# Kernel tuning notes

Hardware: AMD Instinct MI355X
Metric: run time of the kernel (lower is better)

The kernel has to match this reference:

```python
import jax, jax.numpy as jnp
import numpy as np

B, N, D, K = 16, 512, 256, 12  # batch, nodes, node_dim, num edge types (4 arg + 4 arg' + punct +/- + no_edges +/-)
ITERATION_STEPS = 1


def setup_inputs() -> dict:
    key = jax.random.key(0)
    ks = jax.random.split(key, 8)
    node = jax.random.normal(ks[0], (B, N, D), dtype=jnp.float32)
    node_mask = jax.random.randint(ks[1], (B, N), 0, 2, dtype=jnp.int32)
    graphs = jax.random.randint(ks[2], (K, B, N, N), 0, 2, dtype=jnp.int32)
    s = 1.0 / np.sqrt(D)
    Ww = jax.random.normal(ks[3], (1, D), dtype=jnp.float32) * s   # _node_weight_fc
    bw = jnp.zeros((1,), dtype=jnp.float32)
    Ws = jax.random.normal(ks[4], (D, D), dtype=jnp.float32) * s   # _self_node_fc
    bs = jnp.zeros((D,), dtype=jnp.float32)
    Wk = jax.random.normal(ks[5], (K, D, D), dtype=jnp.float32) * s  # 12 bias-free per-edge-type linears
    return {"node": node, "Ww": Ww, "bw": bw, "Ws": Ws, "bs": bs, "Wk": Wk,
            "node_mask": node_mask, "graphs": graphs}


def reference(node, Ww, bw, Ws, bs, Wk, node_mask, graphs):
    dt = node.dtype
    mask = node_mask.astype(dt)
    eye = jnp.eye(N, dtype=dt)
    # dd_graph = mask_row * mask_col * (1 - diag)
    dd = mask[:, None, :] * mask[:, :, None] * (1.0 - eye)          # [B,N,N]
    g = dd[None] * graphs.astype(dt)                                # [K,B,N,N] masked adjacencies
    neigh = g.sum(axis=(0, 3))                                      # [B,N] total neighbor count
    neigh = jnp.where(neigh >= 1, neigh, jnp.ones((), dt))

    all_w = []
    for _ in range(ITERATION_STEPS):
        # (1) node relatedness
        w = jax.nn.sigmoid(node @ Ww.T + bw)[..., 0]                # [B,N]
        all_w.append(w)
        self_info = node @ Ws.T + bs                                # [B,N,D]
        # (2) message propagation for all 12 edge types, batched
        trans = jnp.einsum('bnd,ked->kbne', node, Wk)               # [K,B,N,D] per-type linear (x @ W.T)
        wg = w[None, :, None, :] * g                                # [K,B,N,N] masked node weights
        agg = jnp.einsum('kbmn,kbnd->bmd', wg, trans) / neigh[..., None]
        # (3) update
        node = jax.nn.relu(self_info + agg)

    all_weight = jnp.stack(all_w, axis=1)                           # [B,steps,N]
    return node, all_weight
```

## Files before the change

### kernel.cpp

```cpp
#include <hip/hip_runtime.h>
#include <hip/hip_bf16.h>
#include <math.h>

#define BB 16
#define NN 512
#define DD 256
#define KK 12

typedef __bf16 bf16x8 __attribute__((ext_vector_type(8)));
typedef __bf16 bf16x4 __attribute__((ext_vector_type(4)));
typedef float  f32x4  __attribute__((ext_vector_type(4)));

#define WS_WM     0
#define WS_S      32768
#define WS_NODEBF 65536
#define WS_NODET  4259840
#define WS_WKBF   8454144
#define WS_WSBF   10027008
#define WS_T      10158080

__global__ __launch_bounds__(256) void k1_prep(const float* __restrict__ node,
        const float* __restrict__ Ww, const float* __restrict__ bw,
        const int* __restrict__ node_mask,
        float* __restrict__ wm, __bf16* __restrict__ node_bf,
        float* __restrict__ all_w) {
    int t = threadIdx.x;
    int lane = t & 63;
    int row = blockIdx.x * 4 + (t >> 6);
    const float4 nv = *(const float4*)(node + (size_t)row * DD + lane * 4);
    const float4 wv = *(const float4*)(Ww + lane * 4);
    float dot = nv.x*wv.x + nv.y*wv.y + nv.z*wv.z + nv.w*wv.w;
    #pragma unroll
    for (int off = 32; off > 0; off >>= 1) dot += __shfl_xor(dot, off);
    float w = 1.0f / (1.0f + expf(-(dot + bw[0])));
    int mk = node_mask[row];
    if (lane == 0) {
        wm[row]    = w * (float)mk;
        all_w[row] = w;
    }
    bf16x4 nb = {(__bf16)nv.x, (__bf16)nv.y, (__bf16)nv.z, (__bf16)nv.w};
    *(bf16x4*)(node_bf + (size_t)row * DD + lane * 4) = nb;
}

__global__ __launch_bounds__(256) void k1b_convert(const float* __restrict__ Wk,
        const float* __restrict__ Ws, __bf16* __restrict__ Wk_bf, __bf16* __restrict__ Ws_bf) {
    const int KDD = KK * DD * DD;
    int idx = (blockIdx.x * 256 + threadIdx.x) * 4;
    if (idx < KDD) {
        float4 v = *(const float4*)(Wk + idx);
        bf16x4 o = {(__bf16)v.x, (__bf16)v.y, (__bf16)v.z, (__bf16)v.w};
        *(bf16x4*)(Wk_bf + idx) = o;
    } else {
        int j = idx - KDD;
        if (j < DD * DD) {
            float4 v = *(const float4*)(Ws + j);
            bf16x4 o = {(__bf16)v.x, (__bf16)v.y, (__bf16)v.z, (__bf16)v.w};
            *(bf16x4*)(Ws_bf + j) = o;
        }
    }
}

__global__ __launch_bounds__(256) void k2_transpose(const __bf16* __restrict__ src,
                                                    __bf16* __restrict__ dst) {
    __shared__ __bf16 tile[64][65];
    int bx = blockIdx.x;
    int b = bx >> 5; int rest = bx & 31; int nt = rest >> 2; int dt = rest & 3;
    int n0 = nt * 64, d0 = dt * 64;
    int t = threadIdx.x;
    #pragma unroll
    for (int i = 0; i < 16; i++) {
        int idx = i * 256 + t;
        int n = idx >> 6, d = idx & 63;
        tile[n][d] = src[((size_t)(b * NN + n0 + n)) * DD + d0 + d];
    }
    __syncthreads();
    #pragma unroll
    for (int i = 0; i < 16; i++) {
        int idx = i * 256 + t;
        int d = idx >> 6, n = idx & 63;
        dst[((size_t)(b * DD + d0 + d)) * NN + n0 + n] = tile[n][d];
    }
}

__global__ __launch_bounds__(256) void k3_neigh(const int* __restrict__ graphs,
        const int* __restrict__ node_mask, float* __restrict__ s) {
    int bx = blockIdx.x;
    int b = bx >> 9, m = bx & 511;
    int t = threadIdx.x;
    int j0 = t, j1 = t + 256;
    int mk0 = (j0 != m) ? node_mask[b * NN + j0] : 0;
    int mk1 = (j1 != m) ? node_mask[b * NN + j1] : 0;
    int sum = 0;
    #pragma unroll
    for (int k = 0; k < KK; k++) {
        const int* g = graphs + ((size_t)((k * BB + b) * NN + m)) * NN;
        sum += mk0 * g[j0] + mk1 * g[j1];
    }
    #pragma unroll
    for (int off = 32; off > 0; off >>= 1) sum += __shfl_xor(sum, off);
    __shared__ int partial[4];
    if ((t & 63) == 0) partial[t >> 6] = sum;
    __syncthreads();
    if (t == 0) {
        int tot = partial[0] + partial[1] + partial[2] + partial[3];
        int mm = node_mask[b * NN + m];
        tot *= mm;
        float fn = (float)(tot >= 1 ? tot : 1);
        s[bx] = (float)mm / fn;
    }
}

__global__ __launch_bounds__(256) void k4_stageA(const int* __restrict__ graphs,
        const float* __restrict__ wm, const __bf16* __restrict__ node_t,
        __bf16* __restrict__ T) {
    __shared__ __align__(16) __bf16 Asub[64][72];
    __shared__ __align__(16) __bf16 Bsub[256][72];
    int bx = blockIdx.x;
    int mt = bx & 7;
    int kb = bx >> 3;
    int b = kb & 15;
    int k = kb >> 4;
    int m0 = mt * 64;
    int t = threadIdx.x;
    int lane = t & 63;
    int wave = t >> 6;
    int q = lane >> 4;
    int l16 = lane & 15;

    f32x4 acc[4][4];
    #pragma unroll
    for (int i = 0; i < 4; i++)
        #pragma unroll
        for (int j = 0; j < 4; j++) acc[i][j] = (f32x4){0.f, 0.f, 0.f, 0.f};

    int am = t >> 2;
    int aq = t & 3;
    const int* grow = graphs + ((size_t)((k * BB + b) * NN + m0 + am)) * NN;
    int mg = m0 + am;
    int bd = t >> 2;
    int bq = t & 3;

    for (int n0 = 0; n0 < NN; n0 += 64) {
        #pragma unroll
        for (int i = 0; i < 4; i++) {
            int nbase = n0 + aq * 16 + i * 4;
            int4 g = *(const int4*)(grow + nbase);
            float4 w4 = *(const float4*)(wm + b * NN + nbase);
            __bf16 v0 = (__bf16)((nbase + 0 != mg) ? (float)g.x * w4.x : 0.0f);
            __bf16 v1 = (__bf16)((nbase + 1 != mg) ? (float)g.y * w4.y : 0.0f);
            __bf16 v2 = (__bf16)((nbase + 2 != mg) ? (float)g.z * w4.z : 0.0f);
            __bf16 v3 = (__bf16)((nbase + 3 != mg) ? (float)g.w * w4.w : 0.0f);
            bf16x4 pack = {v0, v1, v2, v3};
            *(bf16x4*)&Asub[am][aq * 16 + i * 4] = pack;
        }
        #pragma unroll
        for (int p = 0; p < 4; p++) {
            int d = bd + p * 64;
            const __bf16* src = node_t + ((size_t)(b * DD + d)) * NN + n0 + bq * 16;
            bf16x8 u0 = *(const bf16x8*)(src);
            bf16x8 u1 = *(const bf16x8*)(src + 8);
            *(bf16x8*)&Bsub[d][bq * 16]     = u0;
            *(bf16x8*)&Bsub[d][bq * 16 + 8] = u1;
        }
        __syncthreads();
        bf16x8 af[4][2], bfr[4][2];
        #pragma unroll
        for (int fm = 0; fm < 4; fm++)
            #pragma unroll
            for (int kk = 0; kk < 2; kk++)
                af[fm][kk] = *(const bf16x8*)&Asub[fm * 16 + l16][kk * 32 + q * 8];
        #pragma unroll
        for (int fd = 0; fd < 4; fd++)
            #pragma unroll
            for (int kk = 0; kk < 2; kk++)
                bfr[fd][kk] = *(const bf16x8*)&Bsub[wave * 64 + fd * 16 + l16][kk * 32 + q * 8];
        #pragma unroll
        for (int fm = 0; fm < 4; fm++)
            #pragma unroll
            for (int fd = 0; fd < 4; fd++)
                #pragma unroll
                for (int kk = 0; kk < 2; kk++)
                    acc[fm][fd] = __builtin_amdgcn_mfma_f32_16x16x32_bf16(
                        af[fm][kk], bfr[fd][kk], acc[fm][fd], 0, 0, 0);
        __syncthreads();
    }
    #pragma unroll
    for (int fm = 0; fm < 4; fm++)
        #pragma unroll
        for (int fd = 0; fd < 4; fd++) {
            int col = wave * 64 + fd * 16 + l16;
            #pragma unroll
            for (int r = 0; r < 4; r++) {
                int m = m0 + fm * 16 + q * 4 + r;
                T[((size_t)((k * BB + b) * NN + m)) * DD + col] = (__bf16)acc[fm][fd][r];
            }
        }
}

__global__ __launch_bounds__(256) void k5_stageB(const __bf16* __restrict__ T,
        const __bf16* __restrict__ Wk_bf, const __bf16* __restrict__ node_bf,
        const __bf16* __restrict__ Ws_bf, const float* __restrict__ bs,
        const float* __restrict__ s, float* __restrict__ out) {
    __shared__ __align__(16) __bf16 AT[32][72];
    __shared__ __align__(16) __bf16 BW[256][72];
    int bx = blockIdx.x;
    int b = bx >> 4;
    int m0 = (bx & 15) * 32;
    int t = threadIdx.x;
    int lane = t & 63;
    int wave = t >> 6;
    int q = lane >> 4;
    int l16 = lane & 15;

    f32x4 acc[2][4];
    #pragma unroll
    for (int i = 0; i < 2; i++)
        #pragma unroll
        for (int j = 0; j < 4; j++) acc[i][j] = (f32x4){0.f, 0.f, 0.f, 0.f};

    int atm = t >> 3; int atc = (t & 7) * 8;
    int bwd = t >> 2; int bwc = (t & 3) * 16;

    for (int k = 0; k < KK; k++) {
        for (int et = 0; et < 4; et++) {
            int e0 = et * 64;
            *(bf16x8*)&AT[atm][atc] =
                *(const bf16x8*)(T + ((size_t)((k * BB + b) * NN + m0 + atm)) * DD + e0 + atc);
            #pragma unroll
            for (int p = 0; p < 4; p++) {
                int d = bwd + p * 64;
                const __bf16* srcp = Wk_bf + ((size_t)(k * DD + d)) * DD + e0 + bwc;
                *(bf16x8*)&BW[d][bwc]     = *(const bf16x8*)(srcp);
                *(bf16x8*)&BW[d][bwc + 8] = *(const bf16x8*)(srcp + 8);
            }
            __syncthreads();
            bf16x8 af[2][2], bfr[4][2];
            #pragma unroll
            for (int fm = 0; fm < 2; fm++)
                #pragma unroll
                for (int kk = 0; kk < 2; kk++)
                    af[fm][kk] = *(const bf16x8*)&AT[fm * 16 + l16][kk * 32 + q * 8];
            #pragma unroll
            for (int fd = 0; fd < 4; fd++)
                #pragma unroll
                for (int kk = 0; kk < 2; kk++)
                    bfr[fd][kk] = *(const bf16x8*)&BW[wave * 64 + fd * 16 + l16][kk * 32 + q * 8];
            #pragma unroll
            for (int fm = 0; fm < 2; fm++)
                #pragma unroll
                for (int fd = 0; fd < 4; fd++)
                    #pragma unroll
                    for (int kk = 0; kk < 2; kk++)
                        acc[fm][fd] = __builtin_amdgcn_mfma_f32_16x16x32_bf16(
                            af[fm][kk], bfr[fd][kk], acc[fm][fd], 0, 0, 0);
            __syncthreads();
        }
    }
    #pragma unroll
    for (int fm = 0; fm < 2; fm++) {
        float sv[4];
        #pragma unroll
        for (int r = 0; r < 4; r++) sv[r] = s[b * NN + m0 + fm * 16 + q * 4 + r];
        #pragma unroll
        for (int fd = 0; fd < 4; fd++)
            #pragma unroll
            for (int r = 0; r < 4; r++) acc[fm][fd][r] *= sv[r];
    }
    for (int et = 0; et < 4; et++) {
        int e0 = et * 64;
        *(bf16x8*)&AT[atm][atc] =
            *(const bf16x8*)(node_bf + ((size_t)(b * NN + m0 + atm)) * DD + e0 + atc);
        #pragma unroll
        for (int p = 0; p < 4; p++) {
            int d = bwd + p * 64;
            const __bf16* srcp = Ws_bf + (size_t)d * DD + e0 + bwc;
            *(bf16x8*)&BW[d][bwc]     = *(const bf16x8*)(srcp);
            *(bf16x8*)&BW[d][bwc + 8] = *(const bf16x8*)(srcp + 8);
        }
        __syncthreads();
        bf16x8 af[2][2], bfr[4][2];
        #pragma unroll
        for (int fm = 0; fm < 2; fm++)
            #pragma unroll
            for (int kk = 0; kk < 2; kk++)
                af[fm][kk] = *(const bf16x8*)&AT[fm * 16 + l16][kk * 32 + q * 8];
        #pragma unroll
        for (int fd = 0; fd < 4; fd++)
            #pragma unroll
            for (int kk = 0; kk < 2; kk++)
                bfr[fd][kk] = *(const bf16x8*)&BW[wave * 64 + fd * 16 + l16][kk * 32 + q * 8];
        #pragma unroll
        for (int fm = 0; fm < 2; fm++)
            #pragma unroll
            for (int fd = 0; fd < 4; fd++)
                #pragma unroll
                for (int kk = 0; kk < 2; kk++)
                    acc[fm][fd] = __builtin_amdgcn_mfma_f32_16x16x32_bf16(
                        af[fm][kk], bfr[fd][kk], acc[fm][fd], 0, 0, 0);
        __syncthreads();
    }
    #pragma unroll
    for (int fm = 0; fm < 2; fm++)
        #pragma unroll
        for (int fd = 0; fd < 4; fd++) {
            int col = wave * 64 + fd * 16 + l16;
            float bsv = bs[col];
            #pragma unroll
            for (int r = 0; r < 4; r++) {
                int m = m0 + fm * 16 + q * 4 + r;
                float v = acc[fm][fd][r] + bsv;
                out[((size_t)(b * NN + m)) * DD + col] = fmaxf(v, 0.0f);
            }
        }
}

extern "C" void kernel_launch(void* const* d_in, const int* in_sizes, int n_in,
                              void* d_out, int out_size, void* d_ws, size_t ws_size,
                              hipStream_t stream) {
    const float* node      = (const float*)d_in[0];
    const float* Ww        = (const float*)d_in[1];
    const float* bw        = (const float*)d_in[2];
    const float* Ws        = (const float*)d_in[3];
    const float* bs        = (const float*)d_in[4];
    const float* Wk        = (const float*)d_in[5];
    const int*   node_mask = (const int*)d_in[6];
    const int*   graphs    = (const int*)d_in[7];
    float* out   = (float*)d_out;
    float* all_w = out + (size_t)BB * NN * DD;

    char* ws = (char*)d_ws;
    float*  wm      = (float*)(ws + WS_WM);
    float*  sbuf    = (float*)(ws + WS_S);
    __bf16* node_bf = (__bf16*)(ws + WS_NODEBF);
    __bf16* node_t  = (__bf16*)(ws + WS_NODET);
    __bf16* Wk_bf   = (__bf16*)(ws + WS_WKBF);
    __bf16* Ws_bf   = (__bf16*)(ws + WS_WSBF);
    __bf16* Tbuf    = (__bf16*)(ws + WS_T);

    k1_prep    <<<2048, 256, 0, stream>>>(node, Ww, bw, node_mask, wm, node_bf, all_w);
    k1b_convert<<< 832, 256, 0, stream>>>(Wk, Ws, Wk_bf, Ws_bf);
    k2_transpose<<<512, 256, 0, stream>>>(node_bf, node_t);
    k3_neigh   <<<8192, 256, 0, stream>>>(graphs, node_mask, sbuf);
    k4_stageA  <<<1536, 256, 0, stream>>>(graphs, wm, node_t, Tbuf);
    k5_stageB  <<< 256, 256, 0, stream>>>(Tbuf, Wk_bf, node_bf, Ws_bf, bs, sbuf, out);
}
```

Measured before the change: 424.6 us.

## Fuse neighbor counting into stage A and retile stage B over contiguous K·D

Removes the separate neighbor-count kernel, which re-read the full int32 graphs tensor. Stage A now counts masked neighbors while it already loads the adjacency rows, treating a nonzero masked node weight as the column mask, and accumulates the counts with atomics into a zeroed buffer. The intermediate T is stored as [b, m, k, d] so stage B can reduce over one contiguous K·D axis with larger 64x128 tiles and a 2x2 wave split. This adds a memset, atomics, and a dependency on the weights never being exactly zero for masked-in nodes.

Measured after the change: 380.9 us. 1.11x faster.

```diff
diff --git a/kernel.cpp b/kernel.cpp
--- a/kernel.cpp
+++ b/kernel.cpp
@@ -12,7 +12,7 @@
 typedef float  f32x4  __attribute__((ext_vector_type(4)));
 
 #define WS_WM     0
-#define WS_S      32768
+#define WS_NCNT   32768
 #define WS_NODEBF 65536
 #define WS_NODET  4259840
 #define WS_WKBF   8454144
@@ -82,37 +82,9 @@
     }
 }
 
-__global__ __launch_bounds__(256) void k3_neigh(const int* __restrict__ graphs,
-        const int* __restrict__ node_mask, float* __restrict__ s) {
-    int bx = blockIdx.x;
-    int b = bx >> 9, m = bx & 511;
-    int t = threadIdx.x;
-    int j0 = t, j1 = t + 256;
-    int mk0 = (j0 != m) ? node_mask[b * NN + j0] : 0;
-    int mk1 = (j1 != m) ? node_mask[b * NN + j1] : 0;
-    int sum = 0;
-    #pragma unroll
-    for (int k = 0; k < KK; k++) {
-        const int* g = graphs + ((size_t)((k * BB + b) * NN + m)) * NN;
-        sum += mk0 * g[j0] + mk1 * g[j1];
-    }
-    #pragma unroll
-    for (int off = 32; off > 0; off >>= 1) sum += __shfl_xor(sum, off);
-    __shared__ int partial[4];
-    if ((t & 63) == 0) partial[t >> 6] = sum;
-    __syncthreads();
-    if (t == 0) {
-        int tot = partial[0] + partial[1] + partial[2] + partial[3];
-        int mm = node_mask[b * NN + m];
-        tot *= mm;
-        float fn = (float)(tot >= 1 ? tot : 1);
-        s[bx] = (float)mm / fn;
-    }
-}
-
 __global__ __launch_bounds__(256) void k4_stageA(const int* __restrict__ graphs,
         const float* __restrict__ wm, const __bf16* __restrict__ node_t,
-        __bf16* __restrict__ T) {
+        __bf16* __restrict__ T, int* __restrict__ ncnt) {
     __shared__ __align__(16) __bf16 Asub[64][72];
     __shared__ __align__(16) __bf16 Bsub[256][72];
     int bx = blockIdx.x;
@@ -139,6 +111,7 @@
     int mg = m0 + am;
     int bd = t >> 2;
     int bq = t & 3;
+    int cnt = 0;
 
     for (int n0 = 0; n0 < NN; n0 += 64) {
         #pragma unroll
@@ -146,10 +119,15 @@
             int nbase = n0 + aq * 16 + i * 4;
             int4 g = *(const int4*)(grow + nbase);
             float4 w4 = *(const float4*)(wm + b * NN + nbase);
-            __bf16 v0 = (__bf16)((nbase + 0 != mg) ? (float)g.x * w4.x : 0.0f);
-            __bf16 v1 = (__bf16)((nbase + 1 != mg) ? (float)g.y * w4.y : 0.0f);
-            __bf16 v2 = (__bf16)((nbase + 2 != mg) ? (float)g.z * w4.z : 0.0f);
-            __bf16 v3 = (__bf16)((nbase + 3 != mg) ? (float)g.w * w4.w : 0.0f);
+            bool v0ok = (nbase + 0 != mg) && (w4.x != 0.0f);
+            bool v1ok = (nbase + 1 != mg) && (w4.y != 0.0f);
+            bool v2ok = (nbase + 2 != mg) && (w4.z != 0.0f);
+            bool v3ok = (nbase + 3 != mg) && (w4.w != 0.0f);
+            cnt += (v0ok ? g.x : 0) + (v1ok ? g.y : 0) + (v2ok ? g.z : 0) + (v3ok ? g.w : 0);
+            __bf16 v0 = (__bf16)(v0ok ? (float)g.x * w4.x : 0.0f);
+            __bf16 v1 = (__bf16)(v1ok ? (float)g.y * w4.y : 0.0f);
+            __bf16 v2 = (__bf16)(v2ok ? (float)g.z * w4.z : 0.0f);
+            __bf16 v3 = (__bf16)(v3ok ? (float)g.w * w4.w : 0.0f);
             bf16x4 pack = {v0, v1, v2, v3};
             *(bf16x4*)&Asub[am][aq * 16 + i * 4] = pack;
         }
@@ -184,6 +162,10 @@
                         af[fm][kk], bfr[fd][kk], acc[fm][fd], 0, 0, 0);
         __syncthreads();
     }
+    cnt += __shfl_xor(cnt, 1);
+    cnt += __shfl_xor(cnt, 2);
+    if ((t & 3) == 0) atomicAdd(&ncnt[b * NN + mg], cnt);
+
     #pragma unroll
     for (int fm = 0; fm < 4; fm++)
         #pragma unroll
@@ -192,7 +174,7 @@
             #pragma unroll
             for (int r = 0; r < 4; r++) {
                 int m = m0 + fm * 16 + q * 4 + r;
-                T[((size_t)((k * BB + b) * NN + m)) * DD + col] = (__bf16)acc[fm][fd][r];
+                T[((size_t)((b * NN + m) * KK + k)) * DD + col] = (__bf16)acc[fm][fd][r];
             }
         }
 }
@@ -200,15 +182,20 @@
 __global__ __launch_bounds__(256) void k5_stageB(const __bf16* __restrict__ T,
         const __bf16* __restrict__ Wk_bf, const __bf16* __restrict__ node_bf,
         const __bf16* __restrict__ Ws_bf, const float* __restrict__ bs,
-        const float* __restrict__ s, float* __restrict__ out) {
-    __shared__ __align__(16) __bf16 AT[32][72];
-    __shared__ __align__(16) __bf16 BW[256][72];
+        const int* __restrict__ ncnt, const int* __restrict__ node_mask,
+        float* __restrict__ out) {
+    __shared__ __align__(16) __bf16 Asub[64][136];
+    __shared__ __align__(16) __bf16 Bsub[128][136];
     int bx = blockIdx.x;
-    int b = bx >> 4;
-    int m0 = (bx & 15) * 32;
+    int rt = bx & 127;
+    int dt = bx >> 7;
+    int b  = rt >> 3;
+    int m0 = (rt & 7) * 64;
     int t = threadIdx.x;
     int lane = t & 63;
     int wave = t >> 6;
+    int wm2 = wave >> 1;
+    int wd2 = wave & 1;
     int q = lane >> 4;
     int l16 = lane & 15;
 
@@ -218,98 +205,100 @@
         #pragma unroll
         for (int j = 0; j < 4; j++) acc[i][j] = (f32x4){0.f, 0.f, 0.f, 0.f};
 
-    int atm = t >> 3; int atc = (t & 7) * 8;
-    int bwd = t >> 2; int bwc = (t & 3) * 16;
-
-    for (int k = 0; k < KK; k++) {
-        for (int et = 0; et < 4; et++) {
-            int e0 = et * 64;
-            *(bf16x8*)&AT[atm][atc] =
-                *(const bf16x8*)(T + ((size_t)((k * BB + b) * NN + m0 + atm)) * DD + e0 + atc);
-            #pragma unroll
-            for (int p = 0; p < 4; p++) {
-                int d = bwd + p * 64;
-                const __bf16* srcp = Wk_bf + ((size_t)(k * DD + d)) * DD + e0 + bwc;
-                *(bf16x8*)&BW[d][bwc]     = *(const bf16x8*)(srcp);
-                *(bf16x8*)&BW[d][bwc + 8] = *(const bf16x8*)(srcp + 8);
-            }
-            __syncthreads();
-            bf16x8 af[2][2], bfr[4][2];
+    int ar = t >> 2; int ac = (t & 3) * 32;
+    int br = t >> 1; int bc = (t & 1) * 64;
+
+    const __bf16* Arow = T + (size_t)(b * NN + m0 + ar) * (KK * DD);
+    const __bf16* Brow0 = Wk_bf + (size_t)(dt * 128 + br) * DD;
+
+    for (int it = 0; it < 24; it++) {
+        int kred0 = it * 128;
+        int k = it >> 1;
+        int e0 = (it & 1) * 128;
+        const __bf16* asrc = Arow + kred0 + ac;
+        #pragma unroll
+        for (int i = 0; i < 4; i++)
+            *(bf16x8*)&Asub[ar][ac + i * 8] = *(const bf16x8*)(asrc + i * 8);
+        const __bf16* bsrc = Brow0 + (size_t)k * DD * DD + e0 + bc;
+        #pragma unroll
+        for (int i = 0; i < 8; i++)
+            *(bf16x8*)&Bsub[br][bc + i * 8] = *(const bf16x8*)(bsrc + i * 8);
+        __syncthreads();
+        #pragma unroll
+        for (int kk = 0; kk < 4; kk++) {
+            bf16x8 af[2], bfr[4];
             #pragma unroll
             for (int fm = 0; fm < 2; fm++)
-                #pragma unroll
-                for (int kk = 0; kk < 2; kk++)
-                    af[fm][kk] = *(const bf16x8*)&AT[fm * 16 + l16][kk * 32 + q * 8];
+                af[fm] = *(const bf16x8*)&Asub[wm2 * 32 + fm * 16 + l16][kk * 32 + q * 8];
             #pragma unroll
             for (int fd = 0; fd < 4; fd++)
-                #pragma unroll
-                for (int kk = 0; kk < 2; kk++)
-                    bfr[fd][kk] = *(const bf16x8*)&BW[wave * 64 + fd * 16 + l16][kk * 32 + q * 8];
+                bfr[fd] = *(const bf16x8*)&Bsub[wd2 * 64 + fd * 16 + l16][kk * 32 + q * 8];
             #pragma unroll
             for (int fm = 0; fm < 2; fm++)
                 #pragma unroll
                 for (int fd = 0; fd < 4; fd++)
-                    #pragma unroll
-                    for (int kk = 0; kk < 2; kk++)
-                        acc[fm][fd] = __builtin_amdgcn_mfma_f32_16x16x32_bf16(
-                            af[fm][kk], bfr[fd][kk], acc[fm][fd], 0, 0, 0);
-            __syncthreads();
-        }
-    }
+                    acc[fm][fd] = __builtin_amdgcn_mfma_f32_16x16x32_bf16(
+                        af[fm], bfr[fd], acc[fm][fd], 0, 0, 0);
+        }
+        __syncthreads();
+    }
+
     #pragma unroll
     for (int fm = 0; fm < 2; fm++) {
-        float sv[4];
-        #pragma unroll
-        for (int r = 0; r < 4; r++) sv[r] = s[b * NN + m0 + fm * 16 + q * 4 + r];
-        #pragma unroll
-        for (int fd = 0; fd < 4; fd++)
-            #pragma unroll
-            for (int r = 0; r < 4; r++) acc[fm][fd][r] *= sv[r];
-    }
-    for (int et = 0; et < 4; et++) {
-        int e0 = et * 64;
-        *(bf16x8*)&AT[atm][atc] =
-            *(const bf16x8*)(node_bf + ((size_t)(b * NN + m0 + atm)) * DD + e0 + atc);
-        #pragma unroll
-        for (int p = 0; p < 4; p++) {
-            int d = bwd + p * 64;
-            const __bf16* srcp = Ws_bf + (size_t)d * DD + e0 + bwc;
-            *(bf16x8*)&BW[d][bwc]     = *(const bf16x8*)(srcp);
-            *(bf16x8*)&BW[d][bwc + 8] = *(const bf16x8*)(srcp + 8);
-        }
-        __syncthreads();
-        bf16x8 af[2][2], bfr[4][2];
-        #pragma unroll
-        for (int fm = 0; fm < 2; fm++)
-            #pragma unroll
-            for (int kk = 0; kk < 2; kk++)
-                af[fm][kk] = *(const bf16x8*)&AT[fm * 16 + l16][kk * 32 + q * 8];
-        #pragma unroll
-        for (int fd = 0; fd < 4; fd++)
-            #pragma unroll
-            for (int kk = 0; kk < 2; kk++)
-                bfr[fd][kk] = *(const bf16x8*)&BW[wave * 64 + fd * 16 + l16][kk * 32 + q * 8];
-        #pragma unroll
-        for (int fm = 0; fm < 2; fm++)
+        #pragma unroll
+        for (int r = 0; r < 4; r++) {
+            int m = m0 + wm2 * 32 + fm * 16 + q * 4 + r;
+            int mk = node_mask[b * NN + m];
+            int c  = ncnt[b * NN + m];
+            float s = (float)mk / (float)(c >= 1 ? c : 1);
+            #pragma unroll
+            for (int fd = 0; fd < 4; fd++) acc[fm][fd][r] *= s;
+        }
+    }
+
+    const __bf16* ArowS = node_bf + (size_t)(b * NN + m0 + ar) * DD;
+    const __bf16* BrowS = Ws_bf + (size_t)(dt * 128 + br) * DD;
+    for (int si = 0; si < 2; si++) {
+        int e0 = si * 128;
+        const __bf16* asrc = ArowS + e0 + ac;
+        #pragma unroll
+        for (int i = 0; i < 4; i++)
+            *(bf16x8*)&Asub[ar][ac + i * 8] = *(const bf16x8*)(asrc + i * 8);
+        const __bf16* bsrc = BrowS + e0 + bc;
+        #pragma unroll
+        for (int i = 0; i < 8; i++)
+            *(bf16x8*)&Bsub[br][bc + i * 8] = *(const bf16x8*)(bsrc + i * 8);
+        __syncthreads();
+        #pragma unroll
+        for (int kk = 0; kk < 4; kk++) {
+            bf16x8 af[2], bfr[4];
+            #pragma unroll
+            for (int fm = 0; fm < 2; fm++)
+                af[fm] = *(const bf16x8*)&Asub[wm2 * 32 + fm * 16 + l16][kk * 32 + q * 8];
             #pragma unroll
             for (int fd = 0; fd < 4; fd++)
+                bfr[fd] = *(const bf16x8*)&Bsub[wd2 * 64 + fd * 16 + l16][kk * 32 + q * 8];
+            #pragma unroll
+            for (int fm = 0; fm < 2; fm++)
                 #pragma unroll
-                for (int kk = 0; kk < 2; kk++)
+                for (int fd = 0; fd < 4; fd++)
                     acc[fm][fd] = __builtin_amdgcn_mfma_f32_16x16x32_bf16(
-                        af[fm][kk], bfr[fd][kk], acc[fm][fd], 0, 0, 0);
-        __syncthreads();
-    }
+                        af[fm], bfr[fd], acc[fm][fd], 0, 0, 0);
+        }
+        __syncthreads();
+    }
+
     #pragma unroll
     for (int fm = 0; fm < 2; fm++)
         #pragma unroll
         for (int fd = 0; fd < 4; fd++) {
-            int col = wave * 64 + fd * 16 + l16;
-            float bsv = bs[col];
+            int d = dt * 128 + wd2 * 64 + fd * 16 + l16;
+            float bsv = bs[d];
             #pragma unroll
             for (int r = 0; r < 4; r++) {
-                int m = m0 + fm * 16 + q * 4 + r;
+                int m = m0 + wm2 * 32 + fm * 16 + q * 4 + r;
                 float v = acc[fm][fd][r] + bsv;
-                out[((size_t)(b * NN + m)) * DD + col] = fmaxf(v, 0.0f);
+                out[((size_t)(b * NN + m)) * DD + d] = fmaxf(v, 0.0f);
             }
         }
 }
@@ -330,17 +319,17 @@
 
     char* ws = (char*)d_ws;
     float*  wm      = (float*)(ws + WS_WM);
-    float*  sbuf    = (float*)(ws + WS_S);
+    int*    ncnt    = (int*)(ws + WS_NCNT);
     __bf16* node_bf = (__bf16*)(ws + WS_NODEBF);
     __bf16* node_t  = (__bf16*)(ws + WS_NODET);
     __bf16* Wk_bf   = (__bf16*)(ws + WS_WKBF);
     __bf16* Ws_bf   = (__bf16*)(ws + WS_WSBF);
     __bf16* Tbuf    = (__bf16*)(ws + WS_T);
 
+    hipMemsetAsync(ncnt, 0, BB * NN * sizeof(int), stream);
     k1_prep    <<<2048, 256, 0, stream>>>(node, Ww, bw, node_mask, wm, node_bf, all_w);
     k1b_convert<<< 832, 256, 0, stream>>>(Wk, Ws, Wk_bf, Ws_bf);
     k2_transpose<<<512, 256, 0, stream>>>(node_bf, node_t);
-    k3_neigh   <<<8192, 256, 0, stream>>>(graphs, node_mask, sbuf);
-    k4_stageA  <<<1536, 256, 0, stream>>>(graphs, wm, node_t, Tbuf);
-    k5_stageB  <<< 256, 256, 0, stream>>>(Tbuf, Wk_bf, node_bf, Ws_bf, bs, sbuf, out);
-}
+    k4_stageA  <<<1536, 256, 0, stream>>>(graphs, wm, node_t, Tbuf, ncnt);
+    k5_stageB  <<< 256, 256, 0, stream>>>(Tbuf, Wk_bf, node_bf, Ws_bf, bs, ncnt, node_mask, out);
+}
```
